# Kernel optimization log

Measured on AMD Instinct MI355X. Metric: run time of the kernel, lower is better.

Reference implementation:

```python
import jax, jax.numpy as jnp
from jax import lax
import numpy as np

# H=W=16 is forced by the module: mask path is a fixed 4x4 lowres map -> ConvTranspose(stride 4) -> 16x16
B, T, H, W = 512, 18, 16, 16
CH, K, D = 128, 8, 128


def setup_inputs():
    key = jax.random.key(0)
    ks = iter(jax.random.split(key, 40))
    def rn(shape, s=0.1):
        return jax.random.normal(next(ks), shape, jnp.float32) * s
    return dict(
        frames=jax.random.uniform(next(ks), (B, T, 1, H, W), jnp.float32),
        enc1_w=rn((CH, 2, 3, 3)), enc1_b=rn((CH,)),
        enc2_w=rn((CH, CH, 4, 4), 0.02), enc2_b=rn((CH,)),
        slot_mu=rn((1, K, D), 0.1),
        to_slot_w=rn((D, CH)), to_slot_b=rn((D,)),
        q_w=rn((D, D)), k_w=rn((D, D)), v_w=rn((D, D)),
        gru_w_ih=rn((3 * D, D)), gru_w_hh=rn((3 * D, D)),
        gru_b_ih=rn((3 * D,)), gru_b_hh=rn((3 * D,)),
        mot1_w=rn((32, D)), mot1_b=rn((32,)),
        mot2_w=rn((2, 32)), mot2_b=rn((2,)),
        mask_w=rn((CH * 16, D)), mask_b=rn((CH * 16,)),
        up_w=rn((K, K, 4, 4)), up_b=rn((K,)),
        res1_w=rn((CH // 2, 1, 3, 3)), res1_b=rn((CH // 2,)),
        res2_w=rn((1, CH // 2, 3, 3)), res2_b=rn((1,)),
    )


def _conv(x, w, b, stride, pad):
    y = lax.conv_general_dilated(x, w, (stride, stride), [(pad, pad), (pad, pad)],
                                 dimension_numbers=('NCHW', 'OIHW', 'NCHW'))
    return y + b[None, :, None, None]


def _gelu(x):
    return jax.nn.gelu(x, approximate=False)  # torch nn.GELU default = exact erf


def reference(frames, enc1_w, enc1_b, enc2_w, enc2_b, slot_mu, to_slot_w, to_slot_b,
              q_w, k_w, v_w, gru_w_ih, gru_w_hh, gru_b_ih, gru_b_hh,
              mot1_w, mot1_b, mot2_w, mot2_b, mask_w, mask_b, up_w, up_b,
              res1_w, res1_b, res2_w, res2_b):
    Bq, Tq = frames.shape[0], frames.shape[1]
    Hh, Ww = frames.shape[-2], frames.shape[-1]
    Kq, Dq = slot_mu.shape[1], slot_mu.shape[2]
    scale = Dq ** 0.5
    # base sampling grid in normalized [-1,1] coords, order (x, y)
    gy, gx = jnp.meshgrid(jnp.linspace(-1.0, 1.0, Hh), jnp.linspace(-1.0, 1.0, Ww), indexing='ij')
    grid = jnp.stack([gx, gy], axis=-1)  # [H,W,2]
    # ConvTranspose2d weight [in,out,kh,kw] -> equivalent forward-conv kernel (swap io, flip spatial)
    up_w_f = jnp.flip(up_w, (2, 3)).transpose(1, 0, 2, 3)

    def gru(x, h):  # torch nn.GRUCell, gate order r,z,n
        gi = x @ gru_w_ih.T + gru_b_ih
        gh = h @ gru_w_hh.T + gru_b_hh
        ir, iz, inn = jnp.split(gi, 3, axis=-1)
        hr, hz, hn = jnp.split(gh, 3, axis=-1)
        r = jax.nn.sigmoid(ir + hr)
        z = jax.nn.sigmoid(iz + hz)
        n = jnp.tanh(inn + r * hn)
        return (1.0 - z) * n + z * h

    def step(slots, pair):
        curr = pair[:, :1]  # [B,1,H,W]
        feat = _gelu(_conv(pair, enc1_w, enc1_b, 1, 1))
        feat = _gelu(_conv(feat, enc2_w, enc2_b, 4, 0))  # [B,CH,H/4,W/4]
        fs = jnp.einsum('bcn,dc->bnd', feat.reshape(Bq, feat.shape[1], -1), to_slot_w) + to_slot_b
        kk = fs @ k_w.T
        vv = fs @ v_w.T
        for _ in range(3):  # fixed 3 slot-attention iterations
            qq = slots @ q_w.T
            attn = jax.nn.softmax(jnp.einsum('bkd,bnd->bkn', qq, kk) / scale, axis=1)
            upd = jnp.einsum('bkn,bnd->bkd', attn, vv)
            slots = gru(upd.reshape(-1, Dq), slots.reshape(-1, Dq)).reshape(Bq, Kq, Dq)
        motion = jnp.tanh(_gelu(slots @ mot1_w.T + mot1_b) @ mot2_w.T + mot2_b) * 4.0  # [B,K,2]
        ml = (slots @ mask_w.T + mask_b).reshape(Bq, Kq, -1, 4, 4).mean(axis=2)  # [B,K,4,4]
        masks = lax.conv_general_dilated(ml, up_w_f, (1, 1), [(3, 3), (3, 3)],
                                         lhs_dilation=(4, 4),
                                         dimension_numbers=('NCHW', 'OIHW', 'NCHW')) + up_b[None, :, None, None]
        masks = jax.nn.softmax(masks, axis=1)  # [B,K,16,16]
        # batched per-slot warp (constant translation per slot); grid_sample bilinear,
        # border padding, align_corners=True
        fsc = motion * 2.0 / jnp.array([Ww, Hh], jnp.float32)
        sg = jnp.clip(grid[None, None] + fsc[:, :, None, None, :], -1.0, 1.0)  # [B,K,H,W,2]
        ix = (sg[..., 0] + 1.0) * 0.5 * (Ww - 1)
        iy = (sg[..., 1] + 1.0) * 0.5 * (Hh - 1)
        x0 = jnp.floor(ix); y0 = jnp.floor(iy)
        wx = ix - x0; wy = iy - y0
        x0i = jnp.clip(x0, 0, Ww - 1).astype(jnp.int32)
        x1i = jnp.clip(x0 + 1, 0, Ww - 1).astype(jnp.int32)
        y0i = jnp.clip(y0, 0, Hh - 1).astype(jnp.int32)
        y1i = jnp.clip(y0 + 1, 0, Hh - 1).astype(jnp.int32)
        img = curr[:, 0]  # [B,H,W]
        bidx = jnp.arange(Bq)[:, None, None, None]
        v00 = img[bidx, y0i, x0i]; v01 = img[bidx, y0i, x1i]
        v10 = img[bidx, y1i, x0i]; v11 = img[bidx, y1i, x1i]
        warped_k = (1 - wy) * ((1 - wx) * v00 + wx * v01) + wy * ((1 - wx) * v10 + wx * v11)  # [B,K,H,W]
        warped = (masks * warped_k).sum(axis=1, keepdims=True)  # [B,1,H,W]
        res = jnp.tanh(_conv(_gelu(_conv(warped - curr, res1_w, res1_b, 1, 1)), res2_w, res2_b, 1, 1)) * 0.1
        pred = jnp.clip(warped + res, 0.0, 1.0)
        return slots, pred

    slots0 = jnp.broadcast_to(slot_mu, (Bq, Kq, Dq))
    # pair = cat([curr, prev], dim=1) for t in 0..T-3
    pairs = jnp.swapaxes(jnp.concatenate([frames[:, 1:Tq - 1], frames[:, :Tq - 2]], axis=2), 0, 1)
    _, preds = lax.scan(step, slots0, pairs)
    return jnp.swapaxes(preds, 0, 1)  # [B,T-2,1,H,W]
```

## Files before the change

### kernel.cpp

```cpp
#include <hip/hip_runtime.h>
#include <math.h>

#define B_TOT 512
#define T_FR  18
#define NSTEP 16

typedef __attribute__((ext_vector_type(8))) short bf16x8;
typedef __attribute__((ext_vector_type(4))) float f32x4;

__device__ __forceinline__ float gelu_f(float x) {
    return 0.5f * x * (1.0f + erff(x * 0.70710678118654752f));
}
__device__ __forceinline__ float sigmoid_f(float x) {
    return 1.0f / (1.0f + expf(-x));
}
__device__ __forceinline__ short f2bf(float x) {
    unsigned int u = __float_as_uint(x);
    return (short)((u + 0x7FFFu + ((u >> 16) & 1u)) >> 16);
}
__device__ __forceinline__ float bflo(unsigned int u) { return __uint_as_float(u << 16); }
__device__ __forceinline__ float bfhi(unsigned int u) { return __uint_as_float(u & 0xffff0000u); }
__device__ __forceinline__ float bf2f(short s) {
    return __uint_as_float(((unsigned int)(unsigned short)s) << 16);
}
__device__ __forceinline__ bf16x8 ld_bf8(const short* p) {
    const short4 lo = *reinterpret_cast<const short4*>(p);
    const short4 hi = *reinterpret_cast<const short4*>(p + 4);
    bf16x8 r;
    r[0] = lo.x; r[1] = lo.y; r[2] = lo.z; r[3] = lo.w;
    r[4] = hi.x; r[5] = hi.y; r[6] = hi.z; r[7] = hi.w;
    return r;
}

#define MFMA(a, bb, c) __builtin_amdgcn_mfma_f32_16x16x32_bf16((a), (bb), (c), 0, 0, 0)

__global__ __launch_bounds__(256) void init_kernel(
    const float* __restrict__ mask_w, const float* __restrict__ mask_b,
    const float* __restrict__ e2w,
    const float* __restrict__ wih, const float* __restrict__ whh,
    const float* __restrict__ qw,
    const float* __restrict__ tsw, const float* __restrict__ tsb,
    const float* __restrict__ kw, const float* __restrict__ vw,
    const float* __restrict__ e1w, const float* __restrict__ e1b,
    float* __restrict__ rmw, float* __restrict__ rmb,
    float* __restrict__ kbf, float* __restrict__ vbf,
    short* __restrict__ w2bf, short* __restrict__ wihbf, short* __restrict__ whhbf,
    short* __restrict__ qwbf, short* __restrict__ kwf, short* __restrict__ vwf,
    short* __restrict__ e1wbf)
{
    const int tid = threadIdx.x, bid = blockIdx.x;
    const int gid = bid * 256 + tid, gstr = gridDim.x * 256;
    const float rscale = 0.08838834764831845f;

    for (int i = gid; i < 128 * 2048; i += gstr) w2bf[i] = f2bf(e2w[i]);
    for (int i = gid; i < 384 * 128; i += gstr) {
        wihbf[i] = f2bf(wih[i]);
        whhbf[i] = f2bf(whh[i]);
    }
    for (int i = gid; i < 128 * 128; i += gstr) qwbf[i] = f2bf(qw[i] * rscale);
    for (int i = gid; i < 128 * 32; i += gstr) {
        const int ci = i >> 5, k = i & 31;
        float v = 0.f;
        if (k < 18) v = e1w[ci * 18 + k];
        else if (k == 18) v = e1b[ci];
        e1wbf[i] = f2bf(v);
    }

    if (bid < 128) {
        const int j = bid;
        if (tid < 128) {
            float s = 0.f;
            for (int d = 0; d < 128; ++d) s += kw[j * 128 + d] * tsw[d * 128 + tid];
            kwf[j * 128 + tid] = f2bf(s);
        } else if (tid == 128) {
            float s = 0.f;
            for (int d = 0; d < 128; ++d) s += kw[j * 128 + d] * tsb[d];
            kbf[j] = s;
        }
    } else if (bid < 256) {
        const int j = bid - 128;
        if (tid < 128) {
            float s = 0.f;
            for (int d = 0; d < 128; ++d) s += vw[j * 128 + d] * tsw[d * 128 + tid];
            vwf[j * 128 + tid] = f2bf(s);
        } else if (tid == 128) {
            float s = 0.f;
            for (int d = 0; d < 128; ++d) s += vw[j * 128 + d] * tsb[d];
            vbf[j] = s;
        }
    }
    if (bid == 256) {
        for (int i = tid; i < 2048; i += 256) {
            const int j = i >> 7, d = i & 127;
            float s = 0.f;
            for (int c = 0; c < 128; ++c) s += mask_w[(c * 16 + j) * 128 + d];
            rmw[i] = s * (1.0f / 128.0f);
        }
        for (int i = tid; i < 16; i += 256) {
            float s = 0.f;
            for (int c = 0; c < 128; ++c) s += mask_b[c * 16 + i];
            rmb[i] = s * (1.0f / 128.0f);
        }
    }
}

#define E_PAIR 0
#define E_F1S  2048
#define E_F2T  22528
#define E_E2B  26752
#define E_KBF  27264
#define E_VBF  27776
#define EPOOLSZ 28288

__global__ __launch_bounds__(256, 2) void encoder_all_kernel(
    const float* __restrict__ frames,
    const short* __restrict__ w2bf, const short* __restrict__ e1wbf,
    const float* __restrict__ e2b_g,
    const short* __restrict__ kwf, const short* __restrict__ vwf,
    const float* __restrict__ kbf_g, const float* __restrict__ vbf_g,
    short* __restrict__ kk_g, short* __restrict__ vv_g)
{
    __shared__ __align__(16) char POOL[EPOOLSZ];
    float* PAIR = (float*)(POOL + E_PAIR);
    short* F1S  = (short*)(POOL + E_F1S);
    short* F2T  = (short*)(POOL + E_F2T);
    float* E2B  = (float*)(POOL + E_E2B);
    float* KBF  = (float*)(POOL + E_KBF);
    float* VBF  = (float*)(POOL + E_VBF);

    const int tid = threadIdx.x;
    const int lane = tid & 63, w = tid >> 6;
    const int g = lane >> 4, cn = lane & 15;
    const int bid = blockIdx.x;
    const int b = bid >> 4, t = bid & 15;
    const int arow = (2 * w) * 16 + cn;
    const int bcol = (4 * (cn >> 2) + (g & 1) * 2) * 20 + 4 * (cn & 3);

    PAIR[tid]       = frames[((size_t)b * T_FR + t + 1) * 256 + tid];
    PAIR[256 + tid] = frames[((size_t)b * T_FR + t) * 256 + tid];
    if (tid < 128) {
        E2B[tid] = e2b_g[tid];
        KBF[tid] = kbf_g[tid];
        VBF[tid] = vbf_g[tid];
    }
    __syncthreads();

    bf16x8 bimj[4];
#pragma unroll
    for (int j = 0; j < 4; ++j) {
        const int pyp = 4 * w + j;
#pragma unroll
        for (int k = 0; k < 8; ++k) {
            const int K = g * 8 + k;
            short v;
            if (K < 18) {
                const int chn = (K >= 9) ? 1 : 0;
                const int q = K - 9 * chn;
                const int ky = q / 3, kx = q - 3 * ky;
                const int yy = pyp + ky - 1, xx = cn + kx - 1;
                const bool ok = (yy >= 0 && yy < 16 && xx >= 0 && xx < 16);
                v = ok ? f2bf(PAIR[chn * 256 + yy * 16 + xx]) : (short)0;
            } else if (K == 18) {
                v = (short)0x3F80;
            } else {
                v = 0;
            }
            bimj[j][k] = v;
        }
    }

    f32x4 acc0 = {0.f, 0.f, 0.f, 0.f};
    f32x4 acc1 = {0.f, 0.f, 0.f, 0.f};
    for (int ch = 0; ch < 4; ++ch) {
        {
            const bf16x8 aw0 = *(const bf16x8*)&e1wbf[(size_t)(ch * 32 + cn) * 32 + g * 8];
            const bf16x8 aw1 = *(const bf16x8*)&e1wbf[(size_t)(ch * 32 + 16 + cn) * 32 + g * 8];
            f32x4 c0[4], c1[4];
#pragma unroll
            for (int j = 0; j < 4; ++j) {
                c0[j] = (f32x4){0.f, 0.f, 0.f, 0.f};
                c1[j] = (f32x4){0.f, 0.f, 0.f, 0.f};
            }
#pragma unroll
            for (int j = 0; j < 4; ++j) {
                c0[j] = MFMA(aw0, bimj[j], c0[j]);
                c1[j] = MFMA(aw1, bimj[j], c1[j]);
            }
#pragma unroll
            for (int j = 0; j < 4; ++j)
#pragma unroll
            for (int r = 0; r < 4; ++r) {
                F1S[(4 * g + r) * 320 + (4 * w + j) * 20 + cn] = f2bf(gelu_f(c0[j][r]));
                F1S[(16 + 4 * g + r) * 320 + (4 * w + j) * 20 + cn] = f2bf(gelu_f(c1[j][r]));
            }
        }
        __syncthreads();
        int rb = (g >> 1) * 320 + bcol;
        int k0 = ch * 512 + g * 8;
        for (int kt = 0; kt < 16; ++kt) {
            const short4 lo = *(const short4*)&F1S[rb];
            const short4 hi = *(const short4*)&F1S[rb + 20];
            bf16x8 bfr;
            bfr[0] = lo.x; bfr[1] = lo.y; bfr[2] = lo.z; bfr[3] = lo.w;
            bfr[4] = hi.x; bfr[5] = hi.y; bfr[6] = hi.z; bfr[7] = hi.w;
            const bf16x8 a0 = *(const bf16x8*)&w2bf[(size_t)arow * 2048 + k0];
            const bf16x8 a1 = *(const bf16x8*)&w2bf[(size_t)(arow + 16) * 2048 + k0];
            acc0 = MFMA(a0, bfr, acc0);
            acc1 = MFMA(a1, bfr, acc1);
            rb += 640; k0 += 32;
        }
        __syncthreads();
    }
    {
        const int cob0 = (2 * w) * 16 + g * 4;
        short4 s0, s1;
        s0.x = f2bf(gelu_f(acc0[0] + E2B[cob0]));
        s0.y = f2bf(gelu_f(acc0[1] + E2B[cob0 + 1]));
        s0.z = f2bf(gelu_f(acc0[2] + E2B[cob0 + 2]));
        s0.w = f2bf(gelu_f(acc0[3] + E2B[cob0 + 3]));
        s1.x = f2bf(gelu_f(acc1[0] + E2B[cob0 + 16]));
        s1.y = f2bf(gelu_f(acc1[1] + E2B[cob0 + 17]));
        s1.z = f2bf(gelu_f(acc1[2] + E2B[cob0 + 18]));
        s1.w = f2bf(gelu_f(acc1[3] + E2B[cob0 + 19]));
        *(short4*)&F2T[cn * 132 + cob0] = s0;
        *(short4*)&F2T[cn * 132 + cob0 + 16] = s1;
    }
    __syncthreads();

    {
        bf16x8 aT[4];
#pragma unroll
        for (int kt = 0; kt < 4; ++kt)
            aT[kt] = ld_bf8(&F2T[cn * 132 + kt * 32 + g * 8]);
        const short* wf = (w >> 1) ? vwf : kwf;
        const int h2 = w & 1;
        f32x4 ac[4];
#pragma unroll
        for (int nt = 0; nt < 4; ++nt) ac[nt] = (f32x4){0.f, 0.f, 0.f, 0.f};
#pragma unroll
        for (int kt = 0; kt < 4; ++kt)
#pragma unroll
        for (int nt = 0; nt < 4; ++nt)
            ac[nt] = MFMA(aT[kt],
                *(const bf16x8*)&wf[(size_t)(h2 * 64 + nt * 16 + cn) * 128 + kt * 32 + g * 8],
                ac[nt]);
        short* dst = (w >> 1) ? vv_g : kk_g;
        const float* bias = (w >> 1) ? VBF : KBF;
        const size_t base = (size_t)bid * 2048;
#pragma unroll
        for (int nt = 0; nt < 4; ++nt) {
            const int j = h2 * 64 + nt * 16 + cn;
            const float bb = bias[j];
#pragma unroll
            for (int r = 0; r < 4; ++r)
                dst[base + (4 * g + r) * 128 + j] = f2bf(ac[nt][r] + bb);
        }
    }
}

#define PO_BIH   0
#define PO_BHH   1536
#define PO_SLOTS 3072
#define PO_SLB0  7168
#define PO_SLB1  11392
#define SCR2     15616
#define T_KK   0
#define T_VV   4224
#define T_QQ   8448
#define T_UPD  12672
#define T_ATT  16896
#define POOLSZ2 (15616 + 17408)

#define LDW(mat, row, kt) (*(const bf16x8*)&mat[(size_t)(row) * 128 + (kt) * 32 + g * 8])

__global__ __launch_bounds__(256, 2) void fused_seq_kernel(
    const float* __restrict__ slot_mu,
    short* __restrict__ kk_g, const short* __restrict__ vv_g,
    const short* __restrict__ qwbf,
    const short* __restrict__ wihbf, const short* __restrict__ whhbf,
    const float* __restrict__ bih_g, const float* __restrict__ bhh_g)
{
    __shared__ __align__(16) char POOL[POOLSZ2];
    const int tid = threadIdx.x;
    const int lane = tid & 63, w = tid >> 6;
    const int g = lane >> 4, cn = lane & 15;
    const int b = blockIdx.x;

    float* BIH = (float*)(POOL + PO_BIH);
    float* BHH = (float*)(POOL + PO_BHH);
    float* SLOTS = (float*)(POOL + PO_SLOTS);
    short* SLB0 = (short*)(POOL + PO_SLB0);
    short* SLB1 = (short*)(POOL + PO_SLB1);

    short* KKl  = (short*)(POOL + SCR2 + T_KK);
    short* VVl  = (short*)(POOL + SCR2 + T_VV);
    short* QQB  = (short*)(POOL + SCR2 + T_QQ);
    short* UPDB = (short*)(POOL + SCR2 + T_UPD);
    float* ATT  = (float*)(POOL + SCR2 + T_ATT);

    for (int i = tid; i < 384; i += 256) { BIH[i] = bih_g[i]; BHH[i] = bhh_g[i]; }
    for (int i = tid; i < 1024; i += 256) {
        const float v = slot_mu[i];
        SLOTS[i] = v;
        SLB0[(i >> 7) * 132 + (i & 127)] = f2bf(v);
    }
    for (int i = tid; i < 8 * 132; i += 256) {
        SLB0[8 * 132 + i] = 0;
        SLB1[8 * 132 + i] = 0;
    }

    const int col0 = 32 * w;
    int cur = 0;
    __syncthreads();

#pragma unroll 1
    for (int t = 0; t < NSTEP; ++t) {
        {
            const size_t base = ((size_t)b * 16 + t) * 2048;
            const int row = tid >> 4, c8 = (tid & 15) * 8;
            const short4 klo = *(const short4*)&kk_g[base + row * 128 + c8];
            const short4 khi = *(const short4*)&kk_g[base + row * 128 + c8 + 4];
            const short4 vlo = *(const short4*)&vv_g[base + row * 128 + c8];
            const short4 vhi = *(const short4*)&vv_g[base + row * 128 + c8 + 4];
            *(short4*)&KKl[row * 132 + c8] = klo;
            *(short4*)&KKl[row * 132 + c8 + 4] = khi;
            *(short4*)&VVl[row * 132 + c8] = vlo;
            *(short4*)&VVl[row * 132 + c8 + 4] = vhi;
        }
        __syncthreads();

        for (int it = 0; it < 3; ++it) {
            short* SLBr = cur ? SLB1 : SLB0;
            short* SLBw = cur ? SLB0 : SLB1;
            bf16x8 aS[4];
#pragma unroll
            for (int kt = 0; kt < 4; ++kt)
                aS[kt] = ld_bf8(&SLBr[cn * 132 + kt * 32 + g * 8]);
            {
                f32x4 qa[2] = {{0.f, 0.f, 0.f, 0.f}, {0.f, 0.f, 0.f, 0.f}};
#pragma unroll
                for (int kt = 0; kt < 4; ++kt)
#pragma unroll
                for (int nt = 0; nt < 2; ++nt)
                    qa[nt] = MFMA(aS[kt], LDW(qwbf, col0 + nt * 16 + cn, kt), qa[nt]);
#pragma unroll
                for (int nt = 0; nt < 2; ++nt)
#pragma unroll
                for (int r = 0; r < 4; ++r)
                    QQB[(4 * g + r) * 132 + col0 + nt * 16 + cn] = f2bf(qa[nt][r]);
            }
            __syncthreads();
            if (tid < 128) {
                const int n = tid >> 3, k = tid & 7;
                float a = 0.f;
                for (int d = 0; d < 128; d += 4) {
                    const uint2 q2 = *(const uint2*)&QQB[k * 132 + d];
                    const uint2 k2 = *(const uint2*)&KKl[n * 132 + d];
                    a += bflo(q2.x) * bflo(k2.x) + bfhi(q2.x) * bfhi(k2.x)
                       + bflo(q2.y) * bflo(k2.y) + bfhi(q2.y) * bfhi(k2.y);
                }
                float m = a;
                m = fmaxf(m, __shfl_xor(m, 1));
                m = fmaxf(m, __shfl_xor(m, 2));
                m = fmaxf(m, __shfl_xor(m, 4));
                const float e = expf(a - m);
                float s = e;
                s += __shfl_xor(s, 1);
                s += __shfl_xor(s, 2);
                s += __shfl_xor(s, 4);
                ATT[k * 16 + n] = e / s;
            }
            __syncthreads();
            {
                const int k8 = tid >> 5, lg = tid & 31;
                float a0 = 0.f, a1 = 0.f, a2 = 0.f, a3 = 0.f;
#pragma unroll
                for (int n = 0; n < 16; ++n) {
                    const float at = ATT[k8 * 16 + n];
                    const uint2 v2 = *(const uint2*)&VVl[n * 132 + 4 * lg];
                    a0 += at * bflo(v2.x); a1 += at * bfhi(v2.x);
                    a2 += at * bflo(v2.y); a3 += at * bfhi(v2.y);
                }
                short4 sv;
                sv.x = f2bf(a0); sv.y = f2bf(a1); sv.z = f2bf(a2); sv.w = f2bf(a3);
                *(short4*)&UPDB[k8 * 132 + 4 * lg] = sv;
            }
            __syncthreads();
            {
                bf16x8 aU[4];
#pragma unroll
                for (int kt = 0; kt < 4; ++kt)
                    aU[kt] = ld_bf8(&UPDB[cn * 132 + kt * 32 + g * 8]);
                f32x4 aR[2], aZ[2], aNIv[2], aNHv[2];
#pragma unroll
                for (int nt = 0; nt < 2; ++nt) {
                    aR[nt] = (f32x4){0.f, 0.f, 0.f, 0.f};
                    aZ[nt] = (f32x4){0.f, 0.f, 0.f, 0.f};
                    aNIv[nt] = (f32x4){0.f, 0.f, 0.f, 0.f};
                    aNHv[nt] = (f32x4){0.f, 0.f, 0.f, 0.f};
                }
#pragma unroll
                for (int nt = 0; nt < 2; ++nt) {
                    const int colj = col0 + nt * 16 + cn;
#pragma unroll
                    for (int kt = 0; kt < 4; ++kt) {
                        aR[nt]   = MFMA(aU[kt], LDW(wihbf, colj, kt), aR[nt]);
                        aR[nt]   = MFMA(aS[kt], LDW(whhbf, colj, kt), aR[nt]);
                        aZ[nt]   = MFMA(aU[kt], LDW(wihbf, 128 + colj, kt), aZ[nt]);
                        aZ[nt]   = MFMA(aS[kt], LDW(whhbf, 128 + colj, kt), aZ[nt]);
                        aNIv[nt] = MFMA(aU[kt], LDW(wihbf, 256 + colj, kt), aNIv[nt]);
                        aNHv[nt] = MFMA(aS[kt], LDW(whhbf, 256 + colj, kt), aNHv[nt]);
                    }
                }
                if (g < 2) {
#pragma unroll
                    for (int nt = 0; nt < 2; ++nt) {
                        const int colj = col0 + nt * 16 + cn;
                        const float br = BIH[colj] + BHH[colj];
                        const float bz = BIH[128 + colj] + BHH[128 + colj];
                        const float bi = BIH[256 + colj], bh = BHH[256 + colj];
#pragma unroll
                        for (int r = 0; r < 4; ++r) {
                            const int kq = 4 * g + r;
                            const float rr = sigmoid_f(aR[nt][r] + br);
                            const float zz = sigmoid_f(aZ[nt][r] + bz);
                            const float nn = tanhf(aNIv[nt][r] + bi + rr * (aNHv[nt][r] + bh));
                            const float hold = SLOTS[kq * 128 + colj];
                            const float hv = (1.f - zz) * nn + zz * hold;
                            SLOTS[kq * 128 + colj] = hv;
                            SLBw[kq * 132 + colj] = f2bf(hv);
                        }
                    }
                }
                __syncthreads();
            }
            cur ^= 1;
        }

        {
            short* SLBr = cur ? SLB1 : SLB0;
            const size_t base = ((size_t)b * 16 + t) * 2048;
            const int i4 = tid * 4;
            const int row = i4 >> 7, col = i4 & 127;
            *(short4*)&kk_g[base + i4] = *(const short4*)&SLBr[row * 132 + col];
        }
        __syncthreads();
    }
}

#define D_SLB  0
#define D_M1W  2112
#define D_RMW  10560
#define D_UPW  14784
#define D_R1W  18880
#define D_R2W  21184
#define D_M1B  23488
#define D_M2W  23616
#define D_M2B  23872
#define D_UPB  23888
#define D_RMB  23920
#define D_R2B  23984
#define D_R1B  24000
#define D_IMG  24256
#define D_MASK 25280
#define D_WARP 33472
#define D_DIFF 34496
#define D_M1O  35520
#define D_MOT  36544
#define D_MLL  36672
#define D_R1S  37184
#define POOLSZ3 45632

__global__ __launch_bounds__(256, 2) void decode_all_kernel(
    const float* __restrict__ frames,
    const short* __restrict__ slots_g,
    const float* __restrict__ m1w_g, const float* __restrict__ m1b_g,
    const float* __restrict__ m2w_g, const float* __restrict__ m2b_g,
    const float* __restrict__ upw_g, const float* __restrict__ upb_g,
    const float* __restrict__ r1w_g, const float* __restrict__ r1b_g,
    const float* __restrict__ r2w_g, const float* __restrict__ r2b_g,
    const float* __restrict__ rmw_g, const float* __restrict__ rmb_g,
    float* __restrict__ out)
{
    __shared__ __align__(16) char POOL[POOLSZ3];
    short* SLB = (short*)(POOL + D_SLB);
    short* M1W = (short*)(POOL + D_M1W);
    short* RMW = (short*)(POOL + D_RMW);
    float* UPW = (float*)(POOL + D_UPW);
    float* R1W = (float*)(POOL + D_R1W);
    float* R2W = (float*)(POOL + D_R2W);
    float* M1B = (float*)(POOL + D_M1B);
    float* M2W = (float*)(POOL + D_M2W);
    float* M2B = (float*)(POOL + D_M2B);
    float* UPB = (float*)(POOL + D_UPB);
    float* RMB = (float*)(POOL + D_RMB);
    float* R2B = (float*)(POOL + D_R2B);
    float* R1B = (float*)(POOL + D_R1B);
    float* IMG = (float*)(POOL + D_IMG);
    float* MASKl = (float*)(POOL + D_MASK);
    float* WARP = (float*)(POOL + D_WARP);
    float* DIFF = (float*)(POOL + D_DIFF);
    float* M1O  = (float*)(POOL + D_M1O);
    float* MOT  = (float*)(POOL + D_MOT);
    float* MLL  = (float*)(POOL + D_MLL);
    short* R1S  = (short*)(POOL + D_R1S);

    const int tid = threadIdx.x;
    const int bid = blockIdx.x;
    const int b = bid >> 4, t = bid & 15;
    const int py = tid >> 4, pxx = tid & 15;

    {
        const size_t base = (size_t)bid * 2048;
        const int i4 = tid * 4;
        const int row = i4 >> 7, col = i4 & 127;
        *(short4*)&SLB[row * 132 + col] = *(const short4*)&slots_g[base + i4];
    }
    for (int i = tid; i < 4096; i += 256)
        M1W[(i >> 7) * 132 + (i & 127)] = f2bf(m1w_g[i]);
    for (int i = tid; i < 2048; i += 256)
        RMW[(i >> 7) * 132 + (i & 127)] = f2bf(rmw_g[i]);
    for (int i = tid; i < 1024; i += 256) UPW[i] = upw_g[i];
    for (int i = tid; i < 576; i += 256) { R1W[i] = r1w_g[i]; R2W[i] = r2w_g[i]; }
    if (tid < 32) M1B[tid] = m1b_g[tid];
    if (tid < 64) { M2W[tid] = m2w_g[tid]; R1B[tid] = r1b_g[tid]; }
    if (tid < 2) M2B[tid] = m2b_g[tid];
    if (tid < 8) UPB[tid] = upb_g[tid];
    if (tid < 16) RMB[tid] = rmb_g[tid];
    if (tid == 0) R2B[0] = r2b_g[0];
    IMG[tid] = frames[((size_t)b * T_FR + t + 1) * 256 + tid];
    __syncthreads();

    {
        const int kq = tid >> 5, c = tid & 31;
        float a = M1B[c];
        for (int d = 0; d < 128; d += 4) {
            const uint2 s2 = *(const uint2*)&SLB[kq * 132 + d];
            const uint2 w2 = *(const uint2*)&M1W[c * 132 + d];
            a += bflo(s2.x) * bflo(w2.x) + bfhi(s2.x) * bfhi(w2.x)
               + bflo(s2.y) * bflo(w2.y) + bfhi(s2.y) * bfhi(w2.y);
        }
        M1O[kq * 32 + c] = gelu_f(a);
    }
    if (tid < 128) {
        const int kq = tid >> 4, j = tid & 15;
        float a = RMB[j];
        for (int d = 0; d < 128; d += 4) {
            const uint2 s2 = *(const uint2*)&SLB[kq * 132 + d];
            const uint2 w2 = *(const uint2*)&RMW[j * 132 + d];
            a += bflo(s2.x) * bflo(w2.x) + bfhi(s2.x) * bfhi(w2.x)
               + bflo(s2.y) * bflo(w2.y) + bfhi(s2.y) * bfhi(w2.y);
        }
        MLL[kq * 16 + j] = a;
    }
    __syncthreads();
    if (tid < 16) {
        const int kq = tid >> 1, e = tid & 1;
        float a = M2B[e];
#pragma unroll
        for (int c = 0; c < 32; ++c) a += M1O[kq * 32 + c] * M2W[e * 32 + c];
        MOT[kq * 2 + e] = tanhf(a) * 4.0f;
    }
    {
        const int jj = (py >> 2) * 4 + (pxx >> 2);
        const int wq = (py & 3) * 4 + (pxx & 3);
#pragma unroll
        for (int ko = 0; ko < 8; ++ko) {
            float a = UPB[ko];
#pragma unroll
            for (int i8 = 0; i8 < 8; ++i8)
                a += MLL[i8 * 16 + jj] * UPW[(i8 * 8 + ko) * 16 + wq];
            MASKl[ko * 256 + tid] = a;
        }
    }
    __syncthreads();
    {
        float m = -1e30f;
#pragma unroll
        for (int kq = 0; kq < 8; ++kq) m = fmaxf(m, MASKl[kq * 256 + tid]);
        float e[8], ssum = 0.f;
#pragma unroll
        for (int kq = 0; kq < 8; ++kq) { e[kq] = expf(MASKl[kq * 256 + tid] - m); ssum += e[kq]; }
        const float inv = 1.f / ssum;
        const float gxv = -1.0f + (2.0f / 15.0f) * pxx;
        const float gyv = -1.0f + (2.0f / 15.0f) * py;
        float wsum = 0.f;
#pragma unroll
        for (int kq = 0; kq < 8; ++kq) {
            const float fx = MOT[kq * 2 + 0] * 0.125f;
            const float fy = MOT[kq * 2 + 1] * 0.125f;
            const float sgx = fminf(fmaxf(gxv + fx, -1.f), 1.f);
            const float sgy = fminf(fmaxf(gyv + fy, -1.f), 1.f);
            const float ix = (sgx + 1.f) * 7.5f;
            const float iy = (sgy + 1.f) * 7.5f;
            const float x0f = floorf(ix), y0f = floorf(iy);
            const float wx = ix - x0f, wy = iy - y0f;
            const int x0 = (int)x0f, y0 = (int)y0f;
            const int x1 = min(x0 + 1, 15), y1 = min(y0 + 1, 15);
            const float v00 = IMG[y0 * 16 + x0], v01 = IMG[y0 * 16 + x1];
            const float v10 = IMG[y1 * 16 + x0], v11 = IMG[y1 * 16 + x1];
            const float val = (1.f - wy) * ((1.f - wx) * v00 + wx * v01) +
                              wy * ((1.f - wx) * v10 + wx * v11);
            wsum += (e[kq] * inv) * val;
        }
        WARP[tid] = wsum;
        DIFF[tid] = wsum - IMG[tid];
    }
    __syncthreads();
    float nbz[9];
#pragma unroll
    for (int ky = 0; ky < 3; ++ky)
#pragma unroll
    for (int kx = 0; kx < 3; ++kx) {
        const int y2 = py + ky - 1, x2 = pxx + kx - 1;
        const bool ok = (y2 >= 0 && y2 < 16 && x2 >= 0 && x2 < 16);
        nbz[ky * 3 + kx] = ok ? DIFF[y2 * 16 + x2] : 0.f;
    }
    float racc = 0.f;
    for (int c0 = 0; c0 < 64; c0 += 16) {
#pragma unroll 4
        for (int cl = 0; cl < 16; ++cl) {
            const int c = c0 + cl;
            float a = R1B[c];
#pragma unroll
            for (int q = 0; q < 9; ++q) a += nbz[q] * R1W[c * 9 + q];
            R1S[cl * 264 + tid] = f2bf(gelu_f(a));
        }
        __syncthreads();
#pragma unroll 4
        for (int cl = 0; cl < 16; ++cl) {
            const float* r2r = &R2W[(c0 + cl) * 9];
#pragma unroll
            for (int ky = 0; ky < 3; ++ky)
#pragma unroll
            for (int kx = 0; kx < 3; ++kx) {
                const int y2 = py + ky - 1, x2 = pxx + kx - 1;
                if (y2 >= 0 && y2 < 16 && x2 >= 0 && x2 < 16)
                    racc += bf2f(R1S[cl * 264 + y2 * 16 + x2]) * r2r[ky * 3 + kx];
            }
        }
        __syncthreads();
    }
    const float resv = tanhf(racc + R2B[0]) * 0.1f;
    const float pred = fminf(fmaxf(WARP[tid] + resv, 0.f), 1.f);
    out[((size_t)b * NSTEP + t) * 256 + tid] = pred;
}

extern "C" void kernel_launch(void* const* d_in, const int* in_sizes, int n_in,
                              void* d_out, int out_size, void* d_ws, size_t ws_size,
                              hipStream_t stream)
{
    const float* frames = (const float*)d_in[0];
    const float* e1w = (const float*)d_in[1];
    const float* e1b = (const float*)d_in[2];
    const float* e2w = (const float*)d_in[3];
    const float* e2b = (const float*)d_in[4];
    const float* slot_mu = (const float*)d_in[5];
    const float* tsw = (const float*)d_in[6];
    const float* tsb = (const float*)d_in[7];
    const float* qw = (const float*)d_in[8];
    const float* kw = (const float*)d_in[9];
    const float* vw = (const float*)d_in[10];
    const float* wih = (const float*)d_in[11];
    const float* whh = (const float*)d_in[12];
    const float* bih = (const float*)d_in[13];
    const float* bhh = (const float*)d_in[14];
    const float* m1w = (const float*)d_in[15];
    const float* m1b = (const float*)d_in[16];
    const float* m2w = (const float*)d_in[17];
    const float* m2b = (const float*)d_in[18];
    const float* maskw = (const float*)d_in[19];
    const float* maskb = (const float*)d_in[20];
    const float* upw = (const float*)d_in[21];
    const float* upb = (const float*)d_in[22];
    const float* r1w = (const float*)d_in[23];
    const float* r1b = (const float*)d_in[24];
    const float* r2w = (const float*)d_in[25];
    const float* r2b = (const float*)d_in[26];

    float* ws = (float*)d_ws;
    float* rmw  = ws + 0;
    float* rmb  = ws + 2048;
    float* kbf  = ws + 2064;
    float* vbf  = ws + 2192;
    short* w2bf  = (short*)(ws + 2320);
    short* wihbf = (short*)(ws + 133392);
    short* whhbf = (short*)(ws + 157968);
    short* qwbf  = (short*)(ws + 182544);
    short* kwf   = (short*)(ws + 190736);
    short* vwf   = (short*)(ws + 198928);
    short* e1wbf = (short*)(ws + 207120);
    short* kk_g  = (short*)(ws + 209168);
    short* vv_g  = (short*)(ws + 209168 + 8388608);

    hipLaunchKernelGGL(init_kernel, dim3(512), dim3(256), 0, stream,
                       maskw, maskb, e2w, wih, whh, qw, tsw, tsb, kw, vw,
                       e1w, e1b,
                       rmw, rmb, kbf, vbf, w2bf, wihbf, whhbf, qwbf, kwf, vwf,
                       e1wbf);
    hipLaunchKernelGGL(encoder_all_kernel, dim3(B_TOT * NSTEP), dim3(256), 0, stream,
                       frames, w2bf, e1wbf, e2b, kwf, vwf, kbf, vbf, kk_g, vv_g);
    hipLaunchKernelGGL(fused_seq_kernel, dim3(B_TOT), dim3(256), 0, stream,
                       slot_mu, kk_g, vv_g, qwbf, wihbf, whhbf, bih, bhh);
    hipLaunchKernelGGL(decode_all_kernel, dim3(B_TOT * NSTEP), dim3(256), 0, stream,
                       frames, kk_g, m1w, m1b, m2w, m2b, upw, upb,
                       r1w, r1b, r2w, r2b, rmw, rmb,
                       (float*)d_out);
}
```

Measured before the change: 1.569 ms.

## Replicate Q and attention per wavefront to drop block-wide barriers

Each wavefront now computes the full Q projection, the attention logits (using an MFMA instead of scalar dot products), the softmax and the attention-weighted V sum into its own private LDS buffers. This removes three __syncthreads per slot-attention iteration and one per time step, so the four waves no longer stall on each other between stages. In exchange each wave does four times the Q projection and the attention work, and LDS use per block roughly doubles, which puts more pressure on the two-blocks-per-CU occupancy target.

```diff
diff --git a/kernel.cpp b/kernel.cpp
--- a/kernel.cpp
+++ b/kernel.cpp
@@ -263,13 +263,12 @@
 #define PO_SLOTS 3072
 #define PO_SLB0  7168
 #define PO_SLB1  11392
-#define SCR2     15616
-#define T_KK   0
-#define T_VV   4224
-#define T_QQ   8448
-#define T_UPD  12672
-#define T_ATT  16896
-#define POOLSZ2 (15616 + 17408)
+#define T_KK     15616
+#define T_VV     19840
+#define T_QQW    24064
+#define T_UPDW   40960
+#define T_ATTW   57856
+#define POOLSZ2  59904
 
 #define LDW(mat, row, kt) (*(const bf16x8*)&mat[(size_t)(row) * 128 + (kt) * 32 + g * 8])
 
@@ -291,12 +290,11 @@
     float* SLOTS = (float*)(POOL + PO_SLOTS);
     short* SLB0 = (short*)(POOL + PO_SLB0);
     short* SLB1 = (short*)(POOL + PO_SLB1);
-
-    short* KKl  = (short*)(POOL + SCR2 + T_KK);
-    short* VVl  = (short*)(POOL + SCR2 + T_VV);
-    short* QQB  = (short*)(POOL + SCR2 + T_QQ);
-    short* UPDB = (short*)(POOL + SCR2 + T_UPD);
-    float* ATT  = (float*)(POOL + SCR2 + T_ATT);
+    short* KKl  = (short*)(POOL + T_KK);
+    short* VVl  = (short*)(POOL + T_VV);
+    short* QQW  = (short*)(POOL + T_QQW) + w * 2112;
+    short* UPDW = (short*)(POOL + T_UPDW) + w * 2112;
+    float* ATTW = (float*)(POOL + T_ATTW) + w * 128;
 
     for (int i = tid; i < 384; i += 256) { BIH[i] = bih_g[i]; BHH[i] = bhh_g[i]; }
     for (int i = tid; i < 1024; i += 256) {
@@ -336,61 +334,72 @@
 #pragma unroll
             for (int kt = 0; kt < 4; ++kt)
                 aS[kt] = ld_bf8(&SLBr[cn * 132 + kt * 32 + g * 8]);
+#pragma unroll
+            for (int nt = 0; nt < 8; ++nt) {
+                f32x4 qa = {0.f, 0.f, 0.f, 0.f};
+#pragma unroll
+                for (int kt = 0; kt < 4; ++kt)
+                    qa = MFMA(aS[kt], LDW(qwbf, nt * 16 + cn, kt), qa);
+#pragma unroll
+                for (int r = 0; r < 4; ++r)
+                    QQW[(4 * g + r) * 132 + nt * 16 + cn] = f2bf(qa[r]);
+            }
             {
-                f32x4 qa[2] = {{0.f, 0.f, 0.f, 0.f}, {0.f, 0.f, 0.f, 0.f}};
+                bf16x8 aQ[4];
 #pragma unroll
                 for (int kt = 0; kt < 4; ++kt)
-#pragma unroll
-                for (int nt = 0; nt < 2; ++nt)
-                    qa[nt] = MFMA(aS[kt], LDW(qwbf, col0 + nt * 16 + cn, kt), qa[nt]);
-#pragma unroll
-                for (int nt = 0; nt < 2; ++nt)
-#pragma unroll
-                for (int r = 0; r < 4; ++r)
-                    QQB[(4 * g + r) * 132 + col0 + nt * 16 + cn] = f2bf(qa[nt][r]);
-            }
-            __syncthreads();
-            if (tid < 128) {
-                const int n = tid >> 3, k = tid & 7;
-                float a = 0.f;
-                for (int d = 0; d < 128; d += 4) {
-                    const uint2 q2 = *(const uint2*)&QQB[k * 132 + d];
-                    const uint2 k2 = *(const uint2*)&KKl[n * 132 + d];
-                    a += bflo(q2.x) * bflo(k2.x) + bfhi(q2.x) * bfhi(k2.x)
-                       + bflo(q2.y) * bflo(k2.y) + bfhi(q2.y) * bfhi(k2.y);
+                    aQ[kt] = ld_bf8(&QQW[cn * 132 + kt * 32 + g * 8]);
+                f32x4 lg = {0.f, 0.f, 0.f, 0.f};
+#pragma unroll
+                for (int kt = 0; kt < 4; ++kt) {
+                    const bf16x8 bK = ld_bf8(&KKl[cn * 132 + kt * 32 + g * 8]);
+                    lg = MFMA(aQ[kt], bK, lg);
                 }
-                float m = a;
-                m = fmaxf(m, __shfl_xor(m, 1));
-                m = fmaxf(m, __shfl_xor(m, 2));
-                m = fmaxf(m, __shfl_xor(m, 4));
-                const float e = expf(a - m);
-                float s = e;
-                s += __shfl_xor(s, 1);
-                s += __shfl_xor(s, 2);
-                s += __shfl_xor(s, 4);
-                ATT[k * 16 + n] = e / s;
-            }
-            __syncthreads();
+                float m = fmaxf(fmaxf(lg[0], lg[1]), fmaxf(lg[2], lg[3]));
+                m = fmaxf(m, __shfl_xor(m, 16));
+                float e0 = expf(lg[0] - m), e1 = expf(lg[1] - m);
+                float e2 = expf(lg[2] - m), e3 = expf(lg[3] - m);
+                float s = e0 + e1 + e2 + e3;
+                s += __shfl_xor(s, 16);
+                const float inv = 1.f / s;
+                if (g < 2) {
+                    ATTW[(4 * g + 0) * 16 + cn] = e0 * inv;
+                    ATTW[(4 * g + 1) * 16 + cn] = e1 * inv;
+                    ATTW[(4 * g + 2) * 16 + cn] = e2 * inv;
+                    ATTW[(4 * g + 3) * 16 + cn] = e3 * inv;
+                }
+            }
             {
-                const int k8 = tid >> 5, lg = tid & 31;
-                float a0 = 0.f, a1 = 0.f, a2 = 0.f, a3 = 0.f;
+                const int kq = lane >> 3, d0 = (lane & 7) * 16;
+                float acc[16];
+#pragma unroll
+                for (int q = 0; q < 16; ++q) acc[q] = 0.f;
 #pragma unroll
                 for (int n = 0; n < 16; ++n) {
-                    const float at = ATT[k8 * 16 + n];
-                    const uint2 v2 = *(const uint2*)&VVl[n * 132 + 4 * lg];
-                    a0 += at * bflo(v2.x); a1 += at * bfhi(v2.x);
-                    a2 += at * bflo(v2.y); a3 += at * bfhi(v2.y);
+                    const float at = ATTW[kq * 16 + n];
+                    const short* vr = &VVl[n * 132 + d0];
+#pragma unroll
+                    for (int q = 0; q < 4; ++q) {
+                        const uint2 v2 = *(const uint2*)&vr[q * 4];
+                        acc[q * 4 + 0] += at * bflo(v2.x);
+                        acc[q * 4 + 1] += at * bfhi(v2.x);
+                        acc[q * 4 + 2] += at * bflo(v2.y);
+                        acc[q * 4 + 3] += at * bfhi(v2.y);
+                    }
                 }
-                short4 sv;
-                sv.x = f2bf(a0); sv.y = f2bf(a1); sv.z = f2bf(a2); sv.w = f2bf(a3);
-                *(short4*)&UPDB[k8 * 132 + 4 * lg] = sv;
-            }
-            __syncthreads();
+#pragma unroll
+                for (int q = 0; q < 4; ++q) {
+                    short4 sv;
+                    sv.x = f2bf(acc[q * 4 + 0]); sv.y = f2bf(acc[q * 4 + 1]);
+                    sv.z = f2bf(acc[q * 4 + 2]); sv.w = f2bf(acc[q * 4 + 3]);
+                    *(short4*)&UPDW[kq * 132 + d0 + q * 4] = sv;
+                }
+            }
             {
                 bf16x8 aU[4];
 #pragma unroll
                 for (int kt = 0; kt < 4; ++kt)
-                    aU[kt] = ld_bf8(&UPDB[cn * 132 + kt * 32 + g * 8]);
+                    aU[kt] = ld_bf8(&UPDW[cn * 132 + kt * 32 + g * 8]);
                 f32x4 aR[2], aZ[2], aNIv[2], aNHv[2];
 #pragma unroll
                 for (int nt = 0; nt < 2; ++nt) {
@@ -444,7 +453,6 @@
             const int row = i4 >> 7, col = i4 & 127;
             *(short4*)&kk_g[base + i4] = *(const short4*)&SLBr[row * 132 + col];
         }
-        __syncthreads();
     }
 }
 
```

Result: slower. 2.306 ms (+47.0%).
